# Kernel optimization log

Measured on AMD Instinct MI355X. Metric: run time of the kernel, lower is better.

## Reference

```python
import jax, jax.numpy as jnp
import numpy as np

N, E, F_IN, F_EXP, H, C = 8192, 65536, 3247, 7993, 3, 512
HC = H * C
NEG_SLOPE = 0.2


def setup_inputs() -> dict:
    key = jax.random.key(0)
    ks = jax.random.split(key, 40)
    s = 0.02
    rnd = lambda k, *sh: (jax.random.normal(k, sh, jnp.float32) * s)
    d = {}
    d['x'] = jax.random.normal(ks[0], (N, F_IN), jnp.float32)
    d['edge_index'] = jax.random.randint(ks[1], (2, E), 0, N, jnp.int32)
    d['exp'] = jax.random.normal(ks[2], (N, F_EXP), jnp.float32)
    # GATv2 layer 1 (in=3247)
    d['w1l'] = rnd(ks[3], F_IN, HC); d['b1l'] = rnd(ks[4], HC)
    d['w1r'] = rnd(ks[5], F_IN, HC); d['b1r'] = rnd(ks[6], HC)
    d['a1'] = rnd(ks[7], H, C);      d['o1'] = rnd(ks[8], HC)
    # GATv2 layer 2 (in=1536)
    d['w2l'] = rnd(ks[9], HC, HC);  d['b2l'] = rnd(ks[10], HC)
    d['w2r'] = rnd(ks[11], HC, HC); d['b2r'] = rnd(ks[12], HC)
    d['a2'] = rnd(ks[13], H, C);     d['o2'] = rnd(ks[14], HC)
    # GATv2 layer 3 (in=1536)
    d['w3l'] = rnd(ks[15], HC, HC); d['b3l'] = rnd(ks[16], HC)
    d['w3r'] = rnd(ks[17], HC, HC); d['b3r'] = rnd(ks[18], HC)
    d['a3'] = rnd(ks[19], H, C);     d['o3'] = rnd(ks[20], HC)
    # encoder: 7993 -> 4000 -> 1500 -> 512
    d['e1w'] = rnd(ks[21], F_EXP, 4000); d['e1b'] = rnd(ks[22], 4000)
    d['e2w'] = rnd(ks[23], 4000, 1500);  d['e2b'] = rnd(ks[24], 1500)
    d['e3w'] = rnd(ks[25], 1500, 512);   d['e3b'] = rnd(ks[26], 512)
    # head: 2048 -> 1024 -> 512 -> 1
    d['l1w'] = rnd(ks[27], HC + 512, 1024); d['l1b'] = rnd(ks[28], 1024)
    d['l2w'] = rnd(ks[29], 1024, 512);      d['l2b'] = rnd(ks[30], 512)
    d['l3w'] = rnd(ks[31], 512, 1);         d['l3b'] = rnd(ks[32], 1)
    return d


def gatv2(h, src, dst, wl, bl, wr, br, att, out_bias):
    # PyG GATv2Conv: e_ij = a^T LeakyReLU(W_l h_j + W_r h_i), softmax over j per target i,
    # out_i = sum_j alpha_ij * (W_l h_j), concat heads, + bias.
    xl = (h @ wl + bl).reshape(N, H, C)
    xr = (h @ wr + br).reshape(N, H, C)
    e = jax.nn.leaky_relu(xl[src] + xr[dst], NEG_SLOPE)      # [E', H, C]
    logit = jnp.einsum('ehc,hc->eh', e, att)                  # [E', H]
    m = jax.ops.segment_max(logit, dst, num_segments=N)       # [N, H]
    p = jnp.exp(logit - m[dst])
    z = jax.ops.segment_sum(p, dst, num_segments=N)
    alpha = p / z[dst]                                        # segment softmax
    out = jax.ops.segment_sum(alpha[:, :, None] * xl[src], dst, num_segments=N)
    return out.reshape(N, HC) + out_bias


def reference(x, edge_index, exp,
              w1l, b1l, w1r, b1r, a1, o1,
              w2l, b2l, w2r, b2r, a2, o2,
              w3l, b3l, w3r, b3r, a3, o3,
              e1w, e1b, e2w, e2b, e3w, e3b,
              l1w, l1b, l2w, l2b, l3w, l3b):
    loops = jnp.arange(N, dtype=edge_index.dtype)
    src = jnp.concatenate([edge_index[0], loops])  # add_self_loops=True (PyG default)
    dst = jnp.concatenate([edge_index[1], loops])
    h = jax.nn.relu(gatv2(x, src, dst, w1l, b1l, w1r, b1r, a1, o1))
    h = jax.nn.relu(gatv2(h, src, dst, w2l, b2l, w2r, b2r, a2, o2))
    h = jax.nn.relu(gatv2(h, src, dst, w3l, b3l, w3r, b3r, a3, o3))
    cell = jax.nn.relu(exp @ e1w + e1b)
    cell = jax.nn.relu(cell @ e2w + e2b)
    cell = cell @ e3w + e3b
    z = jnp.concatenate([h, cell], axis=1)  # [N, 2048]
    z = jax.nn.relu(z @ l1w + l1b)
    z = jax.nn.relu(z @ l2w + l2b)
    return z @ l3w + l3b  # [N, 1]
```

## Files before the change

kernel.cpp:

```cpp
#include <hip/hip_runtime.h>
#include <stdint.h>

#define NN 8192
#define NE 65536
#define ET (NE + NN)
#define F_IN   3247
#define F_IN_P 3264
#define F_EXP   7993
#define F_EXP_P 8000

typedef __attribute__((ext_vector_type(8))) short bf16x8;
typedef __attribute__((ext_vector_type(4))) float f32x4;

typedef const __attribute__((address_space(1))) void gvoid_t;
typedef __attribute__((address_space(3))) void lvoid_t;

__device__ __forceinline__ float bf2f(uint16_t u) {
  union { uint32_t i; float f; } v; v.i = ((uint32_t)u) << 16; return v.f;
}
__device__ __forceinline__ uint16_t f2bf(float f) {
  union { float f; uint32_t i; } v; v.f = f;
  uint32_t r = v.i + 0x7fffu + ((v.i >> 16) & 1u);
  return (uint16_t)(r >> 16);
}

__device__ __forceinline__ void gld_lds16(const void* g, void* l) {
  __builtin_amdgcn_global_load_lds((gvoid_t*)g, (lvoid_t*)l, 16, 0, 0);
}

#define SBAR() __builtin_amdgcn_sched_barrier(0)
#define BARRIER() do { SBAR(); __builtin_amdgcn_s_barrier(); SBAR(); } while (0)
#define VMCNT(n) asm volatile("s_waitcnt vmcnt(" #n ")" ::: "memory")
#define MFMA16(a, b, c) __builtin_amdgcn_mfma_f32_16x16x32_bf16(a, b, c, 0, 0, 0)

__device__ __forceinline__ void stage4(const char* src, char* dst, size_t Kb) {
#pragma unroll
  for (int j = 0; j < 4; ++j)
    gld_lds16(src + (size_t)(j * 64) * Kb, dst + j * 8192);
}

__global__ __launch_bounds__(512, 2)
void gemm256(const uint16_t* __restrict__ A, const uint16_t* __restrict__ Bt,
             const float* __restrict__ bias, int biasN, int relu,
             uint16_t* __restrict__ C, int Kp, int ldc, int nbn)
{
  extern __shared__ char smem[];
  const int tid = threadIdx.x;
  const int w = tid >> 6, lane = tid & 63;
  const int wr = w >> 2, wc = w & 3;
  const int fr = lane & 15, g = lane >> 4;

  const int nwg = (int)gridDim.x;
  const int id = (int)blockIdx.x;
  const int q = nwg >> 3, r = nwg & 7;
  const int xcd = id & 7, idx = id >> 3;
  const int wg = (xcd < r ? xcd * (q + 1) : r * (q + 1) + (xcd - r) * q) + idx;
  const int brow = (wg / nbn) * 256, bcol = (wg % nbn) * 256;

  const size_t Kb = (size_t)Kp * 2;

  const int srow = tid >> 3;
  const int sswz = ((tid & 7) ^ (srow & 7)) * 16;
  const char* pA = (const char*)A + (size_t)(brow + srow) * Kb + sswz;
  const char* pB = (const char*)Bt + (size_t)(bcol + srow) * Kb + sswz;
  char* sA = smem + w * 1024;
  char* sB = smem + 65536 + w * 1024;

  const int sw0 = (g ^ (fr & 7)) * 16;
  const int sw1 = ((g + 4) ^ (fr & 7)) * 16;
  const int arow = (wr * 128 + fr) * 128;
  const int brow_o = (wc * 64 + fr) * 128;

  f32x4 acc[8][4];
#pragma unroll
  for (int m = 0; m < 8; ++m)
#pragma unroll
    for (int n = 0; n < 4; ++n) acc[m][n] = (f32x4){0.f, 0.f, 0.f, 0.f};
  bf16x8 a03[8], a47[8], b01[4], b23[4];

  stage4(pA, sA, Kb);
  stage4(pB, sB, Kb);
  stage4(pA + 128, sA + 32768, Kb);
  stage4(pB + 128, sB + 32768, Kb);
  VMCNT(8);
  BARRIER();
  {
    const char* aB = smem + arow;
#pragma unroll
    for (int m = 0; m < 4; ++m) {
      a03[m * 2]     = *(const bf16x8*)(aB + m * 2048 + sw0);
      a03[m * 2 + 1] = *(const bf16x8*)(aB + m * 2048 + sw1);
    }
  }
  SBAR();

  const int nk = Kp >> 6;
  for (int t = 0; t < nk; ++t) {
    const int buf = (t & 1) << 15;
    const char* aB  = smem + buf + arow;
    const char* bB  = smem + 65536 + buf + brow_o;
    const char* aBn = smem + (buf ^ 32768) + arow;
    const bool nls = (t + 2 < nk);
    const bool nlr = (t + 1 < nk);

    if (nlr) { VMCNT(8); } else { VMCNT(0); }
#pragma unroll
    for (int n = 0; n < 2; ++n) {
      b01[n * 2]     = *(const bf16x8*)(bB + n * 2048 + sw0);
      b01[n * 2 + 1] = *(const bf16x8*)(bB + n * 2048 + sw1);
    }
#pragma unroll
    for (int n = 0; n < 2; ++n) {
      b23[n * 2]     = *(const bf16x8*)(bB + (n + 2) * 2048 + sw0);
      b23[n * 2 + 1] = *(const bf16x8*)(bB + (n + 2) * 2048 + sw1);
    }
    SBAR();
    __builtin_amdgcn_s_setprio(1);
#pragma unroll
    for (int m = 0; m < 4; ++m)
#pragma unroll
      for (int n = 0; n < 2; ++n) {
        acc[m][n] = MFMA16(a03[m * 2],     b01[n * 2],     acc[m][n]);
        acc[m][n] = MFMA16(a03[m * 2 + 1], b01[n * 2 + 1], acc[m][n]);
      }
    __builtin_amdgcn_s_setprio(0);
    BARRIER();

#pragma unroll
    for (int m = 0; m < 4; ++m) {
      a47[m * 2]     = *(const bf16x8*)(aB + (m + 4) * 2048 + sw0);
      a47[m * 2 + 1] = *(const bf16x8*)(aB + (m + 4) * 2048 + sw1);
    }
    SBAR();
    __builtin_amdgcn_s_setprio(1);
#pragma unroll
    for (int m = 0; m < 4; ++m)
#pragma unroll
      for (int n = 0; n < 2; ++n) {
        acc[m][n + 2] = MFMA16(a03[m * 2],     b23[n * 2],     acc[m][n + 2]);
        acc[m][n + 2] = MFMA16(a03[m * 2 + 1], b23[n * 2 + 1], acc[m][n + 2]);
      }
    __builtin_amdgcn_s_setprio(0);
    BARRIER();

    if (nls) stage4(pA + (size_t)(t + 2) * 128, sA + buf, Kb);
#pragma unroll
    for (int n = 0; n < 2; ++n) {
      b01[n * 2]     = *(const bf16x8*)(bB + n * 2048 + sw0);
      b01[n * 2 + 1] = *(const bf16x8*)(bB + n * 2048 + sw1);
    }
    SBAR();
    __builtin_amdgcn_s_setprio(1);
#pragma unroll
    for (int m = 0; m < 4; ++m)
#pragma unroll
      for (int n = 0; n < 2; ++n) {
        acc[m + 4][n + 2] = MFMA16(a47[m * 2],     b23[n * 2],     acc[m + 4][n + 2]);
        acc[m + 4][n + 2] = MFMA16(a47[m * 2 + 1], b23[n * 2 + 1], acc[m + 4][n + 2]);
      }
    __builtin_amdgcn_s_setprio(0);
    BARRIER();

    if (nls)      { VMCNT(8); }
    else if (nlr) { VMCNT(4); }
    if (nlr) {
#pragma unroll
      for (int m = 0; m < 4; ++m) {
        a03[m * 2]     = *(const bf16x8*)(aBn + m * 2048 + sw0);
        a03[m * 2 + 1] = *(const bf16x8*)(aBn + m * 2048 + sw1);
      }
    }
    if (nls) stage4(pB + (size_t)(t + 2) * 128, sB + buf, Kb);
    SBAR();
    __builtin_amdgcn_s_setprio(1);
#pragma unroll
    for (int m = 0; m < 4; ++m)
#pragma unroll
      for (int n = 0; n < 2; ++n) {
        acc[m + 4][n] = MFMA16(a47[m * 2],     b01[n * 2],     acc[m + 4][n]);
        acc[m + 4][n] = MFMA16(a47[m * 2 + 1], b01[n * 2 + 1], acc[m + 4][n]);
      }
    __builtin_amdgcn_s_setprio(0);
    BARRIER();
  }

#pragma unroll
  for (int m = 0; m < 8; ++m) {
    const int row = brow + wr * 128 + m * 16 + g * 4;
#pragma unroll
    for (int n = 0; n < 4; ++n) {
      const int col = bcol + wc * 64 + n * 16 + fr;
      const float bv = (col < biasN) ? bias[col] : 0.f;
#pragma unroll
      for (int j = 0; j < 4; ++j) {
        float v = acc[m][n][j] + bv;
        if (relu) v = fmaxf(v, 0.f);
        C[(size_t)(row + j) * ldc + col] = f2bf(v);
      }
    }
  }
}

__global__ __launch_bounds__(256)
void gemm_bt(const uint16_t* __restrict__ A, const uint16_t* __restrict__ Bt,
             const float* __restrict__ bias, int biasN, int relu,
             uint16_t* __restrict__ C, int Kp, int ldc)
{
  __shared__ uint16_t As[128 * 32];
  __shared__ uint16_t Bs[128 * 32];
  const int tid  = threadIdx.x;
  const int wave = tid >> 6, lane = tid & 63;
  const int brow = blockIdx.x * 128, bcol = blockIdx.y * 128;
  const int wr = wave >> 1, wc = wave & 1;
  const int fr = lane & 15, g = lane >> 4;

  f32x4 acc[4][4];
#pragma unroll
  for (int m = 0; m < 4; ++m)
#pragma unroll
    for (int n = 0; n < 4; ++n) acc[m][n] = (f32x4){0.f, 0.f, 0.f, 0.f};

  const int rA = tid >> 2;
  const int kc = (tid & 3) * 8;
  const uint16_t* aptr = A  + (size_t)(brow + rA) * Kp + kc;
  const uint16_t* bptr = Bt + (size_t)(bcol + rA) * Kp + kc;
  char* ldsA = (char*)As + wave * 1024;
  char* ldsB = (char*)Bs + wave * 1024;
  const size_t rowskip = (size_t)64 * Kp;

  const int nk = Kp >> 5;
  for (int kt = 0; kt < nk; ++kt) {
    __syncthreads();
    gld_lds16(aptr,           ldsA);
    gld_lds16(aptr + rowskip, ldsA + 4096);
    gld_lds16(bptr,           ldsB);
    gld_lds16(bptr + rowskip, ldsB + 4096);
    aptr += 32; bptr += 32;
    __syncthreads();

    bf16x8 af[4], bfr[4];
#pragma unroll
    for (int m = 0; m < 4; ++m)
      af[m] = *(const bf16x8*)&As[(wr * 64 + m * 16 + fr) * 32 + g * 8];
#pragma unroll
    for (int n = 0; n < 4; ++n)
      bfr[n] = *(const bf16x8*)&Bs[(wc * 64 + n * 16 + fr) * 32 + g * 8];
#pragma unroll
    for (int m = 0; m < 4; ++m)
#pragma unroll
      for (int n = 0; n < 4; ++n)
        acc[m][n] = MFMA16(af[m], bfr[n], acc[m][n]);
  }

#pragma unroll
  for (int m = 0; m < 4; ++m) {
    const int row = brow + wr * 64 + m * 16 + g * 4;
#pragma unroll
    for (int n = 0; n < 4; ++n) {
      const int col = bcol + wc * 64 + n * 16 + fr;
      const float bv = (col < biasN) ? bias[col] : 0.f;
#pragma unroll
      for (int j = 0; j < 4; ++j) {
        float v = acc[m][n][j] + bv;
        if (relu) v = fmaxf(v, 0.f);
        C[(size_t)(row + j) * ldc + col] = f2bf(v);
      }
    }
  }
}

__global__ __launch_bounds__(256)
void cvt_pad(const float* __restrict__ in, uint16_t* __restrict__ out, int cols, int colsPad)
{
  const int r = blockIdx.y;
  const int c = (blockIdx.x * 256 + threadIdx.x) * 2;
  if (c >= colsPad) return;
  const float* ip = in + (size_t)r * cols;
  const float v0 = (c < cols)     ? ip[c]     : 0.f;
  const float v1 = (c + 1 < cols) ? ip[c + 1] : 0.f;
  const uint32_t pk = (uint32_t)f2bf(v0) | ((uint32_t)f2bf(v1) << 16);
  *(uint32_t*)(out + (size_t)r * colsPad + c) = pk;
}

__global__ __launch_bounds__(256)
void transpose_w(const float* __restrict__ W, uint16_t* __restrict__ Wt,
                 int K, int N, int Kp, int Np)
{
  __shared__ float t[32][33];
  const int tx = threadIdx.x, ty = threadIdx.y;
  const int k0 = blockIdx.x * 32, n0 = blockIdx.y * 32;
#pragma unroll
  for (int j = 0; j < 4; ++j) {
    const int k = k0 + ty + j * 8, n = n0 + tx;
    t[ty + j * 8][tx] = (k < K && n < N) ? W[(size_t)k * N + n] : 0.f;
  }
  __syncthreads();
#pragma unroll
  for (int j = 0; j < 4; ++j) {
    const int n = n0 + ty + j * 8, k = k0 + tx;
    Wt[(size_t)n * Kp + k] = f2bf(t[tx][ty + j * 8]);
  }
}

__global__ void count_deg(const int* __restrict__ ei, int* __restrict__ counts)
{
  const int e = blockIdx.x * 256 + threadIdx.x;
  if (e >= ET) return;
  const int d = (e < NE) ? ei[NE + e] : (e - NE);
  atomicAdd(&counts[d], 1);
}

__global__ __launch_bounds__(1024)
void scan_deg(const int* __restrict__ counts, int* __restrict__ row_start, int* __restrict__ cursor)
{
  __shared__ int part[1024];
  const int tid = threadIdx.x;
  int loc[8], pre[8], s = 0;
#pragma unroll
  for (int j = 0; j < 8; ++j) { loc[j] = counts[tid * 8 + j]; pre[j] = s; s += loc[j]; }
  part[tid] = s;
  __syncthreads();
  for (int o = 1; o < 1024; o <<= 1) {
    const int v = part[tid];
    const int a = (tid >= o) ? part[tid - o] : 0;
    __syncthreads();
    part[tid] = v + a;
    __syncthreads();
  }
  const int excl = part[tid] - s;
#pragma unroll
  for (int j = 0; j < 8; ++j) {
    const int v = excl + pre[j];
    row_start[tid * 8 + j] = v;
    cursor[tid * 8 + j]    = v;
  }
  if (tid == 1023) row_start[8192] = excl + s;
}

__global__ void scatter_e(const int* __restrict__ ei, int* __restrict__ cursor,
                          int* __restrict__ csr_src, int* __restrict__ csr_dst)
{
  const int e = blockIdx.x * 256 + threadIdx.x;
  if (e >= ET) return;
  const int sx = (e < NE) ? ei[e]      : (e - NE);
  const int d  = (e < NE) ? ei[NE + e] : (e - NE);
  const int pos = atomicAdd(&cursor[d], 1);
  csr_src[pos] = sx;
  csr_dst[pos] = d;
}

__global__ __launch_bounds__(256)
void gat_logits(const uint16_t* __restrict__ xl, const uint16_t* __restrict__ xr,
                const int* __restrict__ csr_src, const int* __restrict__ csr_dst,
                const float* __restrict__ att, float* __restrict__ logit)
{
  const int slot = (blockIdx.x << 2) + (threadIdx.x >> 6);
  if (slot >= ET) return;
  const int lane = threadIdx.x & 63;
  const uint32_t* pl = (const uint32_t*)(xl + (size_t)csr_src[slot] * 1536);
  const uint32_t* pr = (const uint32_t*)(xr + (size_t)csr_dst[slot] * 1536);
  const float2* a2 = (const float2*)att;
  float acc0 = 0.f, acc1 = 0.f, acc2 = 0.f;
#pragma unroll
  for (int it = 0; it < 12; ++it) {
    const int idx = lane + it * 64;
    const uint32_t ul = pl[idx], ur = pr[idx];
    const float2 av = a2[idx];
    float v0 = bf2f((uint16_t)ul)         + bf2f((uint16_t)ur);
    float v1 = bf2f((uint16_t)(ul >> 16)) + bf2f((uint16_t)(ur >> 16));
    v0 = v0 > 0.f ? v0 : 0.2f * v0;
    v1 = v1 > 0.f ? v1 : 0.2f * v1;
    const float p = v0 * av.x + v1 * av.y;
    if (it < 4) acc0 += p; else if (it < 8) acc1 += p; else acc2 += p;
  }
#pragma unroll
  for (int o = 32; o; o >>= 1) {
    acc0 += __shfl_xor(acc0, o);
    acc1 += __shfl_xor(acc1, o);
    acc2 += __shfl_xor(acc2, o);
  }
  if (lane == 0) {
    float* op = logit + (size_t)slot * 3;
    op[0] = acc0; op[1] = acc1; op[2] = acc2;
  }
}

__global__ __launch_bounds__(256)
void gat_aggregate(const float* __restrict__ logit, const int* __restrict__ csr_src,
                   const int* __restrict__ row_start, const uint16_t* __restrict__ xl,
                   const float* __restrict__ ob, uint16_t* __restrict__ out, int ldc)
{
  const int i = blockIdx.x;
  const int tid = threadIdx.x;
  const int s0 = row_start[i], s1 = row_start[i + 1];

  float m0 = -1e30f, m1 = -1e30f, m2 = -1e30f, z0 = 0.f, z1 = 0.f, z2 = 0.f;
  for (int s = s0; s < s1; ++s) {
    const float* lp = logit + (size_t)s * 3;
    float l0 = lp[0], l1 = lp[1], l2 = lp[2];
    float n0 = fmaxf(m0, l0); z0 = z0 * __expf(m0 - n0) + __expf(l0 - n0); m0 = n0;
    float n1 = fmaxf(m1, l1); z1 = z1 * __expf(m1 - n1) + __expf(l1 - n1); m1 = n1;
    float n2 = fmaxf(m2, l2); z2 = z2 * __expf(m2 - n2) + __expf(l2 - n2); m2 = n2;
  }
  const float r0 = 1.f / z0, r1 = 1.f / z1, r2 = 1.f / z2;

  float acc[6] = {0.f, 0.f, 0.f, 0.f, 0.f, 0.f};
  for (int s = s0; s < s1; ++s) {
    const float* lp = logit + (size_t)s * 3;
    const float w0 = __expf(lp[0] - m0) * r0;
    const float w1 = __expf(lp[1] - m1) * r1;
    const float w2 = __expf(lp[2] - m2) * r2;
    const uint16_t* px = xl + (size_t)csr_src[s] * 1536;
    acc[0] += w0 * bf2f(px[tid]);        acc[1] += w0 * bf2f(px[tid + 256]);
    acc[2] += w1 * bf2f(px[tid + 512]);  acc[3] += w1 * bf2f(px[tid + 768]);
    acc[4] += w2 * bf2f(px[tid + 1024]); acc[5] += w2 * bf2f(px[tid + 1280]);
  }
#pragma unroll
  for (int j = 0; j < 6; ++j) {
    const int c = tid + j * 256;
    float v = acc[j] + ob[c];
    v = fmaxf(v, 0.f);
    out[(size_t)i * ldc + c] = f2bf(v);
  }
}

__global__ __launch_bounds__(256)
void final_dot(const uint16_t* __restrict__ z2, const float* __restrict__ w,
               const float* __restrict__ b, float* __restrict__ out)
{
  const int row  = blockIdx.x * 4 + (threadIdx.x >> 6);
  const int lane = threadIdx.x & 63;
  const uint16_t* p = z2 + (size_t)row * 512;
  float s = 0.f;
#pragma unroll
  for (int j = 0; j < 8; ++j) { const int c = lane + j * 64; s += bf2f(p[c]) * w[c]; }
#pragma unroll
  for (int o = 32; o; o >>= 1) s += __shfl_xor(s, o);
  if (lane == 0) out[row] = s + b[0];
}

extern "C" void kernel_launch(void* const* d_in, const int* in_sizes, int n_in,
                              void* d_out, int out_size, void* d_ws, size_t ws_size,
                              hipStream_t stream)
{
  (void)in_sizes; (void)n_in; (void)out_size; (void)ws_size;

  const float* x    = (const float*)d_in[0];
  const int*   ei   = (const int*)  d_in[1];
  const float* expm = (const float*)d_in[2];
  const float* w1l = (const float*)d_in[3];  const float* b1l = (const float*)d_in[4];
  const float* w1r = (const float*)d_in[5];  const float* b1r = (const float*)d_in[6];
  const float* a1  = (const float*)d_in[7];  const float* o1  = (const float*)d_in[8];
  const float* w2l = (const float*)d_in[9];  const float* b2l = (const float*)d_in[10];
  const float* w2r = (const float*)d_in[11]; const float* b2r = (const float*)d_in[12];
  const float* a2  = (const float*)d_in[13]; const float* o2  = (const float*)d_in[14];
  const float* w3l = (const float*)d_in[15]; const float* b3l = (const float*)d_in[16];
  const float* w3r = (const float*)d_in[17]; const float* b3r = (const float*)d_in[18];
  const float* a3  = (const float*)d_in[19]; const float* o3  = (const float*)d_in[20];
  const float* e1w = (const float*)d_in[21]; const float* e1b = (const float*)d_in[22];
  const float* e2w = (const float*)d_in[23]; const float* e2b = (const float*)d_in[24];
  const float* e3w = (const float*)d_in[25]; const float* e3b = (const float*)d_in[26];
  const float* l1w = (const float*)d_in[27]; const float* l1b = (const float*)d_in[28];
  const float* l2w = (const float*)d_in[29]; const float* l2b = (const float*)d_in[30];
  const float* l3w = (const float*)d_in[31]; const float* l3b = (const float*)d_in[32];
  float* out = (float*)d_out;

  hipFuncSetAttribute((const void*)gemm256, hipFuncAttributeMaxDynamicSharedMemorySize, 131072);

  char* ws = (char*)d_ws;
  size_t off = 0;
  auto take = [&](size_t b) { char* p = ws + off; off += (b + 255) & ~(size_t)255; return p; };

  int*      counts    = (int*)take((size_t)NN * 4);
  int*      row_start = (int*)take((size_t)(NN + 1) * 4);
  int*      cursor    = (int*)take((size_t)NN * 4);
  int*      csr_src   = (int*)take((size_t)ET * 4);
  int*      csr_dst   = (int*)take((size_t)ET * 4);
  float*    logits    = (float*)take((size_t)ET * 3 * 4);
  uint16_t* zbuf      = (uint16_t*)take((size_t)NN * 2048 * 2);
  char*     regA      = take((size_t)NN * F_EXP_P * 2);
  char*     regW      = take((size_t)4096 * F_EXP_P * 2);
  char*     regC      = take((size_t)NN * 4096 * 2 + (size_t)NN * 1536 * 2);

  const size_t HCB = (size_t)NN * 1536 * 2;
  uint16_t* xbf   = (uint16_t*)regA;
  uint16_t* expbf = (uint16_t*)regA;
  uint16_t* wT    = (uint16_t*)regW;
  uint16_t* xlb   = (uint16_t*)regC;
  uint16_t* xrb   = (uint16_t*)(regC + HCB);
  uint16_t* hbuf  = (uint16_t*)(regC + 2 * HCB);
  uint16_t* cell1 = (uint16_t*)regC;
  uint16_t* cell2 = (uint16_t*)(regC + (size_t)NN * 4096 * 2);
  uint16_t* zz1   = (uint16_t*)regC;
  uint16_t* zz2   = (uint16_t*)(regC + (size_t)NN * 1024 * 2);

  hipMemsetAsync(counts, 0, (size_t)NN * 4, stream);
  count_deg<<<(ET + 255) / 256, 256, 0, stream>>>(ei, counts);
  scan_deg<<<1, 1024, 0, stream>>>(counts, row_start, cursor);
  scatter_e<<<(ET + 255) / 256, 256, 0, stream>>>(ei, cursor, csr_src, csr_dst);

  cvt_pad<<<dim3((F_IN_P / 2 + 255) / 256, NN), 256, 0, stream>>>(x, xbf, F_IN, F_IN_P);
  transpose_w<<<dim3(F_IN_P / 32, 1536 / 32), dim3(32, 8), 0, stream>>>(w1l, wT, F_IN, 1536, F_IN_P, 1536);
  gemm256<<<32 * 6, 512, 131072, stream>>>(xbf, wT, b1l, 1536, 0, xlb, F_IN_P, 1536, 6);
  transpose_w<<<dim3(F_IN_P / 32, 1536 / 32), dim3(32, 8), 0, stream>>>(w1r, wT, F_IN, 1536, F_IN_P, 1536);
  gemm256<<<32 * 6, 512, 131072, stream>>>(xbf, wT, b1r, 1536, 0, xrb, F_IN_P, 1536, 6);
  gat_logits<<<ET / 4, 256, 0, stream>>>(xlb, xrb, csr_src, csr_dst, a1, logits);
  gat_aggregate<<<NN, 256, 0, stream>>>(logits, csr_src, row_start, xlb, o1, hbuf, 1536);

  transpose_w<<<dim3(48, 48), dim3(32, 8), 0, stream>>>(w2l, wT, 1536, 1536, 1536, 1536);
  gemm256<<<32 * 6, 512, 131072, stream>>>(hbuf, wT, b2l, 1536, 0, xlb, 1536, 1536, 6);
  transpose_w<<<dim3(48, 48), dim3(32, 8), 0, stream>>>(w2r, wT, 1536, 1536, 1536, 1536);
  gemm256<<<32 * 6, 512, 131072, stream>>>(hbuf, wT, b2r, 1536, 0, xrb, 1536, 1536, 6);
  gat_logits<<<ET / 4, 256, 0, stream>>>(xlb, xrb, csr_src, csr_dst, a2, logits);
  gat_aggregate<<<NN, 256, 0, stream>>>(logits, csr_src, row_start, xlb, o2, hbuf, 1536);

  transpose_w<<<dim3(48, 48), dim3(32, 8), 0, stream>>>(w3l, wT, 1536, 1536, 1536, 1536);
  gemm256<<<32 * 6, 512, 131072, stream>>>(hbuf, wT, b3l, 1536, 0, xlb, 1536, 1536, 6);
  transpose_w<<<dim3(48, 48), dim3(32, 8), 0, stream>>>(w3r, wT, 1536, 1536, 1536, 1536);
  gemm256<<<32 * 6, 512, 131072, stream>>>(hbuf, wT, b3r, 1536, 0, xrb, 1536, 1536, 6);
  gat_logits<<<ET / 4, 256, 0, stream>>>(xlb, xrb, csr_src, csr_dst, a3, logits);
  gat_aggregate<<<NN, 256, 0, stream>>>(logits, csr_src, row_start, xlb, o3, zbuf, 2048);

  cvt_pad<<<dim3((F_EXP_P / 2 + 255) / 256, NN), 256, 0, stream>>>(expm, expbf, F_EXP, F_EXP_P);
  transpose_w<<<dim3(F_EXP_P / 32, 4096 / 32), dim3(32, 8), 0, stream>>>(e1w, wT, F_EXP, 4000, F_EXP_P, 4096);
  gemm256<<<32 * 16, 512, 131072, stream>>>(expbf, wT, e1b, 4000, 1, cell1, F_EXP_P, 4096, 16);
  transpose_w<<<dim3(4096 / 32, 1536 / 32), dim3(32, 8), 0, stream>>>(e2w, wT, 4000, 1500, 4096, 1536);
  gemm256<<<32 * 6, 512, 131072, stream>>>(cell1, wT, e2b, 1500, 1, cell2, 4096, 1536, 6);
  transpose_w<<<dim3(1536 / 32, 512 / 32), dim3(32, 8), 0, stream>>>(e3w, wT, 1500, 512, 1536, 512);
  gemm_bt<<<dim3(64, 4), 256, 0, stream>>>(cell2, wT, e3b, 512, 0, zbuf + 1536, 1536, 2048);

  transpose_w<<<dim3(2048 / 32, 1024 / 32), dim3(32, 8), 0, stream>>>(l1w, wT, 2048, 1024, 2048, 1024);
  gemm256<<<32 * 4, 512, 131072, stream>>>(zbuf, wT, l1b, 1024, 1, zz1, 2048, 1024, 4);
  transpose_w<<<dim3(1024 / 32, 512 / 32), dim3(32, 8), 0, stream>>>(l2w, wT, 1024, 512, 1024, 512);
  gemm_bt<<<dim3(64, 4), 256, 0, stream>>>(zz1, wT, l2b, 512, 1, zz2, 1024, 512);
  final_dot<<<NN / 4, 256, 0, stream>>>(zz2, l3w, l3b, out);
}
```

Measured before the change: 1.586 ms.

## Fuse GATv2 left/right projections into one GEMM and vectorize gather kernels

Concatenates the left and right weight matrices and their biases so each GATv2 layer runs a single 8192x3072 GEMM instead of two 1536-wide GEMMs. This doubles the grid to 384 workgroups for better CU fill and removes one launch per layer. The logits kernel now does 16-byte bf16x8 loads with a stride parameter, and the aggregate kernel reads packed pairs and writes 32-bit stores. The GEMM K-loop is unrolled by two via a macro so the buffer offsets become compile-time constants, at the cost of larger code.

After: 1.539 ms. 3.0% less time.

```diff
diff --git a/kernel.cpp b/kernel.cpp
--- a/kernel.cpp
+++ b/kernel.cpp
@@ -38,6 +38,95 @@
   for (int j = 0; j < 4; ++j)
     gld_lds16(src + (size_t)(j * 64) * Kb, dst + j * 8192);
 }
+
+#define KTILE(T, BUF)                                                          \
+  do {                                                                         \
+    const char* aB_  = smem + (BUF) + arow;                                    \
+    const char* bB_  = smem + 65536 + (BUF) + brow_o;                          \
+    const char* aBn_ = smem + ((BUF) ^ 32768) + arow;                          \
+    const bool nls = ((T) + 2 < nk);                                           \
+    const bool nlr = ((T) + 1 < nk);                                           \
+                        \
+    if (nlr) { VMCNT(8); } else { VMCNT(0); }                                  \
+    _Pragma("unroll")                                                          \
+    for (int n = 0; n < 2; ++n) {                                              \
+      b01[n * 2]     = *(const bf16x8*)(bB_ + n * 2048 + sw0);                 \
+      b01[n * 2 + 1] = *(const bf16x8*)(bB_ + n * 2048 + sw1);                 \
+    }                                                                          \
+    _Pragma("unroll")                                                          \
+    for (int n = 0; n < 2; ++n) {                                              \
+      b23[n * 2]     = *(const bf16x8*)(bB_ + (n + 2) * 2048 + sw0);           \
+      b23[n * 2 + 1] = *(const bf16x8*)(bB_ + (n + 2) * 2048 + sw1);           \
+    }                                                                          \
+    SBAR();                                                                    \
+    __builtin_amdgcn_s_setprio(1);                                             \
+    _Pragma("unroll")                                                          \
+    for (int m = 0; m < 4; ++m)                                                \
+      _Pragma("unroll")                                                        \
+      for (int n = 0; n < 2; ++n) {                                            \
+        acc[m][n] = MFMA16(a03[m * 2],     b01[n * 2],     acc[m][n]);         \
+        acc[m][n] = MFMA16(a03[m * 2 + 1], b01[n * 2 + 1], acc[m][n]);         \
+      }                                                                        \
+    __builtin_amdgcn_s_setprio(0);                                             \
+    BARRIER();                                                                 \
+                                        \
+    _Pragma("unroll")                                                          \
+    for (int m = 0; m < 4; ++m) {                                              \
+      a47[m * 2]     = *(const bf16x8*)(aB_ + (m + 4) * 2048 + sw0);           \
+      a47[m * 2 + 1] = *(const bf16x8*)(aB_ + (m + 4) * 2048 + sw1);           \
+    }                                                                          \
+    SBAR();                                                                    \
+    __builtin_amdgcn_s_setprio(1);                                             \
+    _Pragma("unroll")                                                          \
+    for (int m = 0; m < 4; ++m)                                                \
+      _Pragma("unroll")                                                        \
+      for (int n = 0; n < 2; ++n) {                                            \
+        acc[m][n + 2] = MFMA16(a03[m * 2],     b23[n * 2],     acc[m][n + 2]); \
+        acc[m][n + 2] = MFMA16(a03[m * 2 + 1], b23[n * 2 + 1], acc[m][n + 2]); \
+      }                                                                        \
+    __builtin_amdgcn_s_setprio(0);                                             \
+    BARRIER();                                                                 \
+                       \
+    if (nls) stage4(pA + (size_t)((T) + 2) * 128, sA + (BUF), Kb);             \
+    _Pragma("unroll")                                                          \
+    for (int n = 0; n < 2; ++n) {                                              \
+      b01[n * 2]     = *(const bf16x8*)(bB_ + n * 2048 + sw0);                 \
+      b01[n * 2 + 1] = *(const bf16x8*)(bB_ + n * 2048 + sw1);                 \
+    }                                                                          \
+    SBAR();                                                                    \
+    __builtin_amdgcn_s_setprio(1);                                             \
+    _Pragma("unroll")                                                          \
+    for (int m = 0; m < 4; ++m)                                                \
+      _Pragma("unroll")                                                        \
+      for (int n = 0; n < 2; ++n) {                                            \
+        acc[m + 4][n + 2] = MFMA16(a47[m * 2],     b23[n * 2],     acc[m + 4][n + 2]); \
+        acc[m + 4][n + 2] = MFMA16(a47[m * 2 + 1], b23[n * 2 + 1], acc[m + 4][n + 2]); \
+      }                                                                        \
+    __builtin_amdgcn_s_setprio(0);                                             \
+    BARRIER();                                                                 \
+       \
+    if (nls)      { VMCNT(8); }                                                \
+    else if (nlr) { VMCNT(4); }                                                \
+    if (nlr) {                                                                 \
+      _Pragma("unroll")                                                        \
+      for (int m = 0; m < 4; ++m) {                                            \
+        a03[m * 2]     = *(const bf16x8*)(aBn_ + m * 2048 + sw0);              \
+        a03[m * 2 + 1] = *(const bf16x8*)(aBn_ + m * 2048 + sw1);              \
+      }                                                                        \
+    }                                                                          \
+    if (nls) stage4(pB + (size_t)((T) + 2) * 128, sB + (BUF), Kb);             \
+    SBAR();                                                                    \
+    __builtin_amdgcn_s_setprio(1);                                             \
+    _Pragma("unroll")                                                          \
+    for (int m = 0; m < 4; ++m)                                                \
+      _Pragma("unroll")                                                        \
+      for (int n = 0; n < 2; ++n) {                                            \
+        acc[m + 4][n] = MFMA16(a47[m * 2],     b01[n * 2],     acc[m + 4][n]); \
+        acc[m + 4][n] = MFMA16(a47[m * 2 + 1], b01[n * 2 + 1], acc[m + 4][n]); \
+      }                                                                        \
+    __builtin_amdgcn_s_setprio(0);                                             \
+    BARRIER();                                                                 \
+  } while (0)
 
 __global__ __launch_bounds__(512, 2)
 void gemm256(const uint16_t* __restrict__ A, const uint16_t* __restrict__ Bt,
@@ -95,93 +184,9 @@
   SBAR();
 
   const int nk = Kp >> 6;
-  for (int t = 0; t < nk; ++t) {
-    const int buf = (t & 1) << 15;
-    const char* aB  = smem + buf + arow;
-    const char* bB  = smem + 65536 + buf + brow_o;
-    const char* aBn = smem + (buf ^ 32768) + arow;
-    const bool nls = (t + 2 < nk);
-    const bool nlr = (t + 1 < nk);
-
-    if (nlr) { VMCNT(8); } else { VMCNT(0); }
-#pragma unroll
-    for (int n = 0; n < 2; ++n) {
-      b01[n * 2]     = *(const bf16x8*)(bB + n * 2048 + sw0);
-      b01[n * 2 + 1] = *(const bf16x8*)(bB + n * 2048 + sw1);
-    }
-#pragma unroll
-    for (int n = 0; n < 2; ++n) {
-      b23[n * 2]     = *(const bf16x8*)(bB + (n + 2) * 2048 + sw0);
-      b23[n * 2 + 1] = *(const bf16x8*)(bB + (n + 2) * 2048 + sw1);
-    }
-    SBAR();
-    __builtin_amdgcn_s_setprio(1);
-#pragma unroll
-    for (int m = 0; m < 4; ++m)
-#pragma unroll
-      for (int n = 0; n < 2; ++n) {
-        acc[m][n] = MFMA16(a03[m * 2],     b01[n * 2],     acc[m][n]);
-        acc[m][n] = MFMA16(a03[m * 2 + 1], b01[n * 2 + 1], acc[m][n]);
-      }
-    __builtin_amdgcn_s_setprio(0);
-    BARRIER();
-
-#pragma unroll
-    for (int m = 0; m < 4; ++m) {
-      a47[m * 2]     = *(const bf16x8*)(aB + (m + 4) * 2048 + sw0);
-      a47[m * 2 + 1] = *(const bf16x8*)(aB + (m + 4) * 2048 + sw1);
-    }
-    SBAR();
-    __builtin_amdgcn_s_setprio(1);
-#pragma unroll
-    for (int m = 0; m < 4; ++m)
-#pragma unroll
-      for (int n = 0; n < 2; ++n) {
-        acc[m][n + 2] = MFMA16(a03[m * 2],     b23[n * 2],     acc[m][n + 2]);
-        acc[m][n + 2] = MFMA16(a03[m * 2 + 1], b23[n * 2 + 1], acc[m][n + 2]);
-      }
-    __builtin_amdgcn_s_setprio(0);
-    BARRIER();
-
-    if (nls) stage4(pA + (size_t)(t + 2) * 128, sA + buf, Kb);
-#pragma unroll
-    for (int n = 0; n < 2; ++n) {
-      b01[n * 2]     = *(const bf16x8*)(bB + n * 2048 + sw0);
-      b01[n * 2 + 1] = *(const bf16x8*)(bB + n * 2048 + sw1);
-    }
-    SBAR();
-    __builtin_amdgcn_s_setprio(1);
-#pragma unroll
-    for (int m = 0; m < 4; ++m)
-#pragma unroll
-      for (int n = 0; n < 2; ++n) {
-        acc[m + 4][n + 2] = MFMA16(a47[m * 2],     b23[n * 2],     acc[m + 4][n + 2]);
-        acc[m + 4][n + 2] = MFMA16(a47[m * 2 + 1], b23[n * 2 + 1], acc[m + 4][n + 2]);
-      }
-    __builtin_amdgcn_s_setprio(0);
-    BARRIER();
-
-    if (nls)      { VMCNT(8); }
-    else if (nlr) { VMCNT(4); }
-    if (nlr) {
-#pragma unroll
-      for (int m = 0; m < 4; ++m) {
-        a03[m * 2]     = *(const bf16x8*)(aBn + m * 2048 + sw0);
-        a03[m * 2 + 1] = *(const bf16x8*)(aBn + m * 2048 + sw1);
-      }
-    }
-    if (nls) stage4(pB + (size_t)(t + 2) * 128, sB + buf, Kb);
-    SBAR();
-    __builtin_amdgcn_s_setprio(1);
-#pragma unroll
-    for (int m = 0; m < 4; ++m)
-#pragma unroll
-      for (int n = 0; n < 2; ++n) {
-        acc[m + 4][n] = MFMA16(a47[m * 2],     b01[n * 2],     acc[m + 4][n]);
-        acc[m + 4][n] = MFMA16(a47[m * 2 + 1], b01[n * 2 + 1], acc[m + 4][n]);
-      }
-    __builtin_amdgcn_s_setprio(0);
-    BARRIER();
+  for (int t = 0; t < nk; t += 2) {
+    KTILE(t, 0);
+    if (t + 1 < nk) KTILE(t + 1, 32768);
   }
 
 #pragma unroll
@@ -302,6 +307,14 @@
   }
 }
 
+__global__ void concat_bias(const float* __restrict__ bl, const float* __restrict__ br,
+                            float* __restrict__ out)
+{
+  const int i = blockIdx.x * 256 + threadIdx.x;
+  if (i < 1536) out[i] = bl[i];
+  else if (i < 3072) out[i] = br[i - 1536];
+}
+
 __global__ void count_deg(const int* __restrict__ ei, int* __restrict__ counts)
 {
   const int e = blockIdx.x * 256 + threadIdx.x;
@@ -350,44 +363,46 @@
 }
 
 __global__ __launch_bounds__(256)
-void gat_logits(const uint16_t* __restrict__ xl, const uint16_t* __restrict__ xr,
+void gat_logits(const uint16_t* __restrict__ xl, const uint16_t* __restrict__ xr, int ld,
                 const int* __restrict__ csr_src, const int* __restrict__ csr_dst,
                 const float* __restrict__ att, float* __restrict__ logit)
 {
   const int slot = (blockIdx.x << 2) + (threadIdx.x >> 6);
-  if (slot >= ET) return;
   const int lane = threadIdx.x & 63;
-  const uint32_t* pl = (const uint32_t*)(xl + (size_t)csr_src[slot] * 1536);
-  const uint32_t* pr = (const uint32_t*)(xr + (size_t)csr_dst[slot] * 1536);
-  const float2* a2 = (const float2*)att;
-  float acc0 = 0.f, acc1 = 0.f, acc2 = 0.f;
-#pragma unroll
-  for (int it = 0; it < 12; ++it) {
-    const int idx = lane + it * 64;
-    const uint32_t ul = pl[idx], ur = pr[idx];
-    const float2 av = a2[idx];
-    float v0 = bf2f((uint16_t)ul)         + bf2f((uint16_t)ur);
-    float v1 = bf2f((uint16_t)(ul >> 16)) + bf2f((uint16_t)(ur >> 16));
-    v0 = v0 > 0.f ? v0 : 0.2f * v0;
-    v1 = v1 > 0.f ? v1 : 0.2f * v1;
-    const float p = v0 * av.x + v1 * av.y;
-    if (it < 4) acc0 += p; else if (it < 8) acc1 += p; else acc2 += p;
+  const bf16x8* pl = (const bf16x8*)(xl + (size_t)csr_src[slot] * ld);
+  const bf16x8* pr = (const bf16x8*)(xr + (size_t)csr_dst[slot] * ld);
+  float hacc[3];
+#pragma unroll
+  for (int h = 0; h < 3; ++h) {
+    const bf16x8 vl = pl[h * 64 + lane];
+    const bf16x8 vr = pr[h * 64 + lane];
+    const float4 a0 = *(const float4*)(att + h * 512 + lane * 8);
+    const float4 a1 = *(const float4*)(att + h * 512 + lane * 8 + 4);
+    float s = 0.f;
+#pragma unroll
+    for (int j = 0; j < 8; ++j) {
+      float v = bf2f((uint16_t)vl[j]) + bf2f((uint16_t)vr[j]);
+      v = v > 0.f ? v : 0.2f * v;
+      const float a = (j < 4) ? ((const float*)&a0)[j] : ((const float*)&a1)[j - 4];
+      s += v * a;
+    }
+    hacc[h] = s;
   }
 #pragma unroll
   for (int o = 32; o; o >>= 1) {
-    acc0 += __shfl_xor(acc0, o);
-    acc1 += __shfl_xor(acc1, o);
-    acc2 += __shfl_xor(acc2, o);
+    hacc[0] += __shfl_xor(hacc[0], o);
+    hacc[1] += __shfl_xor(hacc[1], o);
+    hacc[2] += __shfl_xor(hacc[2], o);
   }
   if (lane == 0) {
     float* op = logit + (size_t)slot * 3;
-    op[0] = acc0; op[1] = acc1; op[2] = acc2;
+    op[0] = hacc[0]; op[1] = hacc[1]; op[2] = hacc[2];
   }
 }
 
 __global__ __launch_bounds__(256)
 void gat_aggregate(const float* __restrict__ logit, const int* __restrict__ csr_src,
-                   const int* __restrict__ row_start, const uint16_t* __restrict__ xl,
+                   const int* __restrict__ row_start, const uint16_t* __restrict__ xl, int ldx,
                    const float* __restrict__ ob, uint16_t* __restrict__ out, int ldc)
 {
   const int i = blockIdx.x;
@@ -404,23 +419,30 @@
   }
   const float r0 = 1.f / z0, r1 = 1.f / z1, r2 = 1.f / z2;
 
-  float acc[6] = {0.f, 0.f, 0.f, 0.f, 0.f, 0.f};
+  float accl[3], acch[3];
+#pragma unroll
+  for (int h = 0; h < 3; ++h) { accl[h] = 0.f; acch[h] = 0.f; }
   for (int s = s0; s < s1; ++s) {
     const float* lp = logit + (size_t)s * 3;
-    const float w0 = __expf(lp[0] - m0) * r0;
-    const float w1 = __expf(lp[1] - m1) * r1;
-    const float w2 = __expf(lp[2] - m2) * r2;
-    const uint16_t* px = xl + (size_t)csr_src[s] * 1536;
-    acc[0] += w0 * bf2f(px[tid]);        acc[1] += w0 * bf2f(px[tid + 256]);
-    acc[2] += w1 * bf2f(px[tid + 512]);  acc[3] += w1 * bf2f(px[tid + 768]);
-    acc[4] += w2 * bf2f(px[tid + 1024]); acc[5] += w2 * bf2f(px[tid + 1280]);
-  }
-#pragma unroll
-  for (int j = 0; j < 6; ++j) {
-    const int c = tid + j * 256;
-    float v = acc[j] + ob[c];
-    v = fmaxf(v, 0.f);
-    out[(size_t)i * ldc + c] = f2bf(v);
+    float wv[3];
+    wv[0] = __expf(lp[0] - m0) * r0;
+    wv[1] = __expf(lp[1] - m1) * r1;
+    wv[2] = __expf(lp[2] - m2) * r2;
+    const uint32_t* px = (const uint32_t*)(xl + (size_t)csr_src[s] * ldx);
+#pragma unroll
+    for (int h = 0; h < 3; ++h) {
+      const uint32_t u = px[h * 256 + tid];
+      accl[h] += wv[h] * bf2f((uint16_t)u);
+      acch[h] += wv[h] * bf2f((uint16_t)(u >> 16));
+    }
+  }
+#pragma unroll
+  for (int h = 0; h < 3; ++h) {
+    const int c = h * 512 + 2 * tid;
+    float v0 = fmaxf(accl[h] + ob[c], 0.f);
+    float v1 = fmaxf(acch[h] + ob[c + 1], 0.f);
+    const uint32_t pk = (uint32_t)f2bf(v0) | ((uint32_t)f2bf(v1) << 16);
+    *(uint32_t*)(out + (size_t)i * ldc + c) = pk;
   }
 }
 
@@ -477,18 +499,19 @@
   int*      csr_src   = (int*)take((size_t)ET * 4);
   int*      csr_dst   = (int*)take((size_t)ET * 4);
   float*    logits    = (float*)take((size_t)ET * 3 * 4);
+  float*    bc1       = (float*)take(3072 * 4);
+  float*    bc2       = (float*)take(3072 * 4);
+  float*    bc3       = (float*)take(3072 * 4);
   uint16_t* zbuf      = (uint16_t*)take((size_t)NN * 2048 * 2);
   char*     regA      = take((size_t)NN * F_EXP_P * 2);
   char*     regW      = take((size_t)4096 * F_EXP_P * 2);
   char*     regC      = take((size_t)NN * 4096 * 2 + (size_t)NN * 1536 * 2);
 
-  const size_t HCB = (size_t)NN * 1536 * 2;
   uint16_t* xbf   = (uint16_t*)regA;
   uint16_t* expbf = (uint16_t*)regA;
   uint16_t* wT    = (uint16_t*)regW;
-  uint16_t* xlb   = (uint16_t*)regC;
-  uint16_t* xrb   = (uint16_t*)(regC + HCB);
-  uint16_t* hbuf  = (uint16_t*)(regC + 2 * HCB);
+  uint16_t* xlr   = (uint16_t*)regC;
+  uint16_t* hbuf  = (uint16_t*)(regC + (size_t)NN * 3072 * 2);
   uint16_t* cell1 = (uint16_t*)regC;
   uint16_t* cell2 = (uint16_t*)(regC + (size_t)NN * 4096 * 2);
   uint16_t* zz1   = (uint16_t*)regC;
@@ -498,28 +521,28 @@
   count_deg<<<(ET + 255) / 256, 256, 0, stream>>>(ei, counts);
   scan_deg<<<1, 1024, 0, stream>>>(counts, row_start, cursor);
   scatter_e<<<(ET + 255) / 256, 256, 0, stream>>>(ei, cursor, csr_src, csr_dst);
+  concat_bias<<<12, 256, 0, stream>>>(b1l, b1r, bc1);
+  concat_bias<<<12, 256, 0, stream>>>(b2l, b2r, bc2);
+  concat_bias<<<12, 256, 0, stream>>>(b3l, b3r, bc3);
 
   cvt_pad<<<dim3((F_IN_P / 2 + 255) / 256, NN), 256, 0, stream>>>(x, xbf, F_IN, F_IN_P);
   transpose_w<<<dim3(F_IN_P / 32, 1536 / 32), dim3(32, 8), 0, stream>>>(w1l, wT, F_IN, 1536, F_IN_P, 1536);
-  gemm256<<<32 * 6, 512, 131072, stream>>>(xbf, wT, b1l, 1536, 0, xlb, F_IN_P, 1536, 6);
-  transpose_w<<<dim3(F_IN_P / 32, 1536 / 32), dim3(32, 8), 0, stream>>>(w1r, wT, F_IN, 1536, F_IN_P, 1536);
-  gemm256<<<32 * 6, 512, 131072, stream>>>(xbf, wT, b1r, 1536, 0, xrb, F_IN_P, 1536, 6);
-  gat_logits<<<ET / 4, 256, 0, stream>>>(xlb, xrb, csr_src, csr_dst, a1, logits);
-  gat_aggregate<<<NN, 256, 0, stream>>>(logits, csr_src, row_start, xlb, o1, hbuf, 1536);
+  transpose_w<<<dim3(F_IN_P / 32, 1536 / 32), dim3(32, 8), 0, stream>>>(w1r, wT + (size_t)1536 * F_IN_P, F_IN, 1536, F_IN_P, 1536);
+  gemm256<<<32 * 12, 512, 131072, stream>>>(xbf, wT, bc1, 3072, 0, xlr, F_IN_P, 3072, 12);
+  gat_logits<<<ET / 4, 256, 0, stream>>>(xlr, xlr + 1536, 3072, csr_src, csr_dst, a1, logits);
+  gat_aggregate<<<NN, 256, 0, stream>>>(logits, csr_src, row_start, xlr, 3072, o1, hbuf, 1536);
 
   transpose_w<<<dim3(48, 48), dim3(32, 8), 0, stream>>>(w2l, wT, 1536, 1536, 1536, 1536);
-  gemm256<<<32 * 6, 512, 131072, stream>>>(hbuf, wT, b2l, 1536, 0, xlb, 1536, 1536, 6);
-  transpose_w<<<dim3(48, 48), dim3(32, 8), 0, stream>>>(w2r, wT, 1536, 1536, 1536, 1536);
-  gemm256<<<32 * 6, 512, 131072, stream>>>(hbuf, wT, b2r, 1536, 0, xrb, 1536, 1536, 6);
-  gat_logits<<<ET / 4, 256, 0, stream>>>(xlb, xrb, csr_src, csr_dst, a2, logits);
-  gat_aggregate<<<NN, 256, 0, stream>>>(logits, csr_src, row_start, xlb, o2, hbuf, 1536);
+  transpose_w<<<dim3(48, 48), dim3(32, 8), 0, stream>>>(w2r, wT + (size_t)1536 * 1536, 1536, 1536, 1536, 1536);
+  gemm256<<<32 * 12, 512, 131072, stream>>>(hbuf, wT, bc2, 3072, 0, xlr, 1536, 3072, 12);
+  gat_logits<<<ET / 4, 256, 0, stream>>>(xlr, xlr + 1536, 3072, csr_src, csr_dst, a2, logits);
+  gat_aggregate<<<NN, 256, 0, stream>>>(logits, csr_src, row_start, xlr, 3072, o2, hbuf, 1536);
 
   transpose_w<<<dim3(48, 48), dim3(32, 8), 0, stream>>>(w3l, wT, 1536, 1536, 1536, 1536);
-  gemm256<<<32 * 6, 512, 131072, stream>>>(hbuf, wT, b3l, 1536, 0, xlb, 1536, 1536, 6);
-  transpose_w<<<dim3(48, 48), dim3(32, 8), 0, stream>>>(w3r, wT, 1536, 1536, 1536, 1536);
-  gemm256<<<32 * 6, 512, 131072, stream>>>(hbuf, wT, b3r, 1536, 0, xrb, 1536, 1536, 6);
-  gat_logits<<<ET / 4, 256, 0, stream>>>(xlb, xrb, csr_src, csr_dst, a3, logits);
-  gat_aggregate<<<NN, 256, 0, stream>>>(logits, csr_src, row_start, xlb, o3, zbuf, 2048);
+  transpose_w<<<dim3(48, 48), dim3(32, 8), 0, stream>>>(w3r, wT + (size_t)1536 * 1536, 1536, 1536, 1536, 1536);
+  gemm256<<<32 * 12, 512, 131072, stream>>>(hbuf, wT, bc3, 3072, 0, xlr, 1536, 3072, 12);
+  gat_logits<<<ET / 4, 256, 0, stream>>>(xlr, xlr + 1536, 3072, csr_src, csr_dst, a3, logits);
+  gat_aggregate<<<NN, 256, 0, stream>>>(logits, csr_src, row_start, xlr, 3072, o3, zbuf, 2048);
 
   cvt_pad<<<dim3((F_EXP_P / 2 + 255) / 256, NN), 256, 0, stream>>>(expm, expbf, F_EXP, F_EXP_P);
   transpose_w<<<dim3(F_EXP_P / 32, 4096 / 32), dim3(32, 8), 0, stream>>>(e1w, wT, F_EXP, 4000, F_EXP_P, 4096);
```
